# Performance work log

Measured on AMD Instinct MI355X. Metric: run time of the kernel, lower is better.

The kernel has to match this reference:

```python
import jax, jax.numpy as jnp
import numpy as np

N = 100000      # nodes
E = 3200000     # edges (avg degree 32)
F_IN = 500      # PubMed node features
H = 16          # hidden
C = 3           # PubMed classes


def setup_inputs() -> dict:
    key = jax.random.key(0)
    k1, k2, k3, k4, k5, k6 = jax.random.split(key, 6)
    x = jax.random.normal(k1, (N, F_IN), dtype=jnp.float32)
    edge_index = jax.random.randint(k2, (2, E), 0, N, dtype=jnp.int32)
    # GCNConv weights (glorot-ish scale) and zero biases
    W1 = jax.random.normal(k3, (F_IN, H), dtype=jnp.float32) * np.float32(np.sqrt(2.0 / (F_IN + H)))
    b1 = jnp.zeros((H,), dtype=jnp.float32)
    W2 = jax.random.normal(k4, (H, C), dtype=jnp.float32) * np.float32(np.sqrt(2.0 / (H + C)))
    b2 = jnp.zeros((C,), dtype=jnp.float32)
    return {"x": x, "W1": W1, "b1": b1, "W2": W2, "b2": b2, "edge_index": edge_index}


def gcn_layer(x, W, b, src, dst, n):
    # GCNConv: linear transform, add self-loops, symmetric degree normalization, scatter-add
    h = x @ W                                   # [N, F_out]
    loop = jnp.arange(n, dtype=src.dtype)
    s = jnp.concatenate([src, loop])            # [E+N]
    d = jnp.concatenate([dst, loop])            # [E+N]
    deg = jax.ops.segment_sum(jnp.ones_like(d, dtype=h.dtype), d, num_segments=n)
    dinv = jax.lax.rsqrt(jnp.maximum(deg, 1.0))  # deg >= 1 due to self-loops
    norm = dinv[s] * dinv[d]                    # [E+N]
    out = jax.ops.segment_sum(h[s] * norm[:, None], d, num_segments=n)
    return out + b


def reference(x, W1, b1, W2, b2, edge_index):
    src, dst = edge_index[0], edge_index[1]
    h = gcn_layer(x, W1, b1, src, dst, N)
    h = jax.nn.relu(h)
    # F.dropout in eval mode (reference is deterministic) is identity
    out = gcn_layer(h, W2, b2, src, dst, N)
    return jax.nn.log_softmax(out, axis=1)
```

## Files before the change

kernel.cpp:

```cpp
#include <hip/hip_runtime.h>
#include <hip/hip_fp16.h>
#include <math.h>

#define N_NODES 100000
#define N_EDGES 3200000
#define F_INF   500
#define H_DIM   16
#define C_DIM   3

#define NB      782
#define CAP     4608
#define GPAD    16
#define EPB     16384
#define NBLK_PART ((N_EDGES + EPB - 1) / EPB)

#define OFF_GCUR  0
#define OFF_DINV  12512
#define OFF_PAIRS 112512
#define OFF_ROWS  3715968
#define OFF_H1H   3816064
#define OFF_H2H   4616064

typedef float        f32x4 __attribute__((ext_vector_type(4)));
typedef unsigned int u32x4 __attribute__((ext_vector_type(4)));
typedef unsigned int u32x2 __attribute__((ext_vector_type(2)));

template <typename T>
__device__ inline T ntload(const T* p) { return __builtin_nontemporal_load(p); }
template <typename T>
__device__ inline void ntstore(T* p, T v) { __builtin_nontemporal_store(v, p); }

__device__ inline float2 h2f(unsigned u) {
    __half2 h = *reinterpret_cast<__half2*>(&u);
    return __half22float2(h);
}
__device__ inline unsigned f2h(float a, float b) {
    __half2 h = __floats2half2_rn(a, b);
    return *reinterpret_cast<unsigned*>(&h);
}

__global__ void k_init(int* __restrict__ gcur) {
    int b = blockIdx.x * 256 + threadIdx.x;
    if (b < NB) gcur[b * GPAD] = b * CAP;
}

__global__ __launch_bounds__(512) void k_part(const int* __restrict__ src,
                                              const int* __restrict__ dst,
                                              int* __restrict__ gcur,
                                              unsigned int* __restrict__ pairs) {
    __shared__ unsigned sbuf[EPB];
    __shared__ int lcnt[NB];
    __shared__ int lbase[NB];
    __shared__ int lstart[NB];
    __shared__ int lrank[NB];
    __shared__ int wtot[8];
    int t = threadIdx.x;
    int wid = t >> 6, lane = t & 63;
    int e0 = blockIdx.x * EPB;
    for (int i = t; i < NB; i += 512) { lcnt[i] = 0; lrank[i] = 0; }
    __syncthreads();
    for (int i = t; i < EPB; i += 512) {
        int e = e0 + i;
        if (e < N_EDGES) atomicAdd(&lcnt[ntload(dst + e) >> 7], 1);
    }
    __syncthreads();
    for (int b = t; b < NB; b += 512) {
        int c = lcnt[b];
        lbase[b] = c ? atomicAdd(&gcur[b * GPAD], c) : 0;
    }
    {
        int b0 = wid * 128 + lane * 2;
        int c0 = (b0 < NB) ? lcnt[b0] : 0;
        int c1 = (b0 + 1 < NB) ? lcnt[b0 + 1] : 0;
        int s = c0 + c1;
        int inc = s;
        for (int o = 1; o < 64; o <<= 1) { int y = __shfl_up(inc, o); if (lane >= o) inc += y; }
        if (lane == 63) wtot[wid] = inc;
        int excl = inc - s;
        if (b0 < NB) lstart[b0] = excl;
        if (b0 + 1 < NB) lstart[b0 + 1] = excl + c0;
    }
    __syncthreads();
    if (t == 0) { int r = 0; for (int w = 0; w < 8; ++w) { int v = wtot[w]; wtot[w] = r; r += v; } }
    __syncthreads();
    {
        int b0 = wid * 128 + lane * 2;
        int add = wtot[wid];
        if (b0 < NB) lstart[b0] += add;
        if (b0 + 1 < NB) lstart[b0 + 1] += add;
    }
    __syncthreads();
    for (int i = t; i < EPB; i += 512) {
        int e = e0 + i;
        if (e < N_EDGES) {
            int d = ntload(dst + e);
            int b = d >> 7;
            int r = atomicAdd(&lrank[b], 1);
            sbuf[lstart[b] + r] = ((unsigned)ntload(src + e) << 7) | (unsigned)(d & 127);
        }
    }
    __syncthreads();
    for (int b = wid; b < NB; b += 8) {
        int c = lcnt[b], ls = lstart[b], gb = lbase[b];
        int lim = (b + 1) * CAP;
        for (int i = lane; i < c; i += 64) {
            int pos = gb + i;
            if (pos < lim)
                pairs[pos] = sbuf[ls + i];
        }
    }
}

__global__ __launch_bounds__(512) void k_sort(unsigned int* __restrict__ pairs,
                                              const int* __restrict__ gcur,
                                              float* __restrict__ dinv,
                                              int* __restrict__ rows) {
    __shared__ unsigned sbuf[CAP];
    __shared__ unsigned sout[CAP];
    __shared__ int cnt[128];
    __shared__ int start[128];
    __shared__ int rank[128];
    int b = blockIdx.x, t = threadIdx.x;
    if (t < 128) { cnt[t] = 0; rank[t] = 0; }
    __syncthreads();
    int base = b * CAP;
    int n = min(gcur[b * GPAD] - base, CAP);
    for (int i = t; i < n; i += 512) {
        unsigned p = ntload(pairs + base + i);
        sbuf[i] = p;
        atomicAdd(&cnt[p & 127], 1);
    }
    __syncthreads();
    if (t < 64) {
        int c0 = cnt[2 * t], c1 = cnt[2 * t + 1];
        int s = c0 + c1;
        int inc = s;
        for (int o = 1; o < 64; o <<= 1) { int y = __shfl_up(inc, o); if (t >= o) inc += y; }
        int excl = inc - s;
        start[2 * t] = excl;
        start[2 * t + 1] = excl + c0;
        rows[b * 128 + 2 * t]     = (excl << 16) | c0;
        rows[b * 128 + 2 * t + 1] = ((excl + c0) << 16) | c1;
    }
    if (t >= 64 && t < 192) {
        int l = t - 64;
        int v = b * 128 + l;
        if (v < N_NODES) dinv[v] = rsqrtf((float)(cnt[l] + 1));
    }
    __syncthreads();
    for (int i = t; i < n; i += 512) {
        unsigned p = sbuf[i];
        int k = p & 127;
        int r = atomicAdd(&rank[k], 1);
        sout[start[k] + r] = p;
    }
    __syncthreads();
    for (int i = t; i < n; i += 512) ntstore(pairs + base + i, sout[i]);
}

#define KTILE 60
#define KSTRIDE 61
__global__ __launch_bounds__(256) void k_gemm1(const float* __restrict__ x,
                                               const float* __restrict__ W1,
                                               const float* __restrict__ dinv,
                                               unsigned int* __restrict__ h1h) {
    __shared__ float xs[256 * KSTRIDE];
    int t = threadIdx.x;
    int row0 = blockIdx.x * 256;
    int row = row0 + t;
    float acc[16];
#pragma unroll
    for (int j = 0; j < 16; ++j) acc[j] = 0.f;
    int rr = t >> 4;
    int cc = t & 15;
    for (int k0 = 0; k0 < F_INF; k0 += KTILE) {
        int kw = F_INF - k0; if (kw > KTILE) kw = KTILE;
        int nf4 = kw >> 2;
        __syncthreads();
#pragma unroll
        for (int s = 0; s < 16; ++s) {
            int r = s * 16 + rr;
            int gr = row0 + r;
            if (cc < nf4 && gr < N_NODES) {
                f32x4 v = ntload(reinterpret_cast<const f32x4*>(x + (size_t)gr * F_INF + k0 + cc * 4));
                float* q = xs + r * KSTRIDE + cc * 4;
                q[0] = v.x; q[1] = v.y; q[2] = v.z; q[3] = v.w;
            }
        }
        __syncthreads();
        if (row < N_NODES) {
            for (int kk = 0; kk < kw; ++kk) {
                float xv = xs[t * KSTRIDE + kk];
                const float* Wk = W1 + (k0 + kk) * 16;
#pragma unroll
                for (int j = 0; j < 16; ++j) acc[j] = fmaf(xv, Wk[j], acc[j]);
            }
        }
    }
    if (row < N_NODES) {
        float dv = dinv[row];
        u32x4 o0, o1;
        o0.x = f2h(dv * acc[0],  dv * acc[1]);  o0.y = f2h(dv * acc[2],  dv * acc[3]);
        o0.z = f2h(dv * acc[4],  dv * acc[5]);  o0.w = f2h(dv * acc[6],  dv * acc[7]);
        o1.x = f2h(dv * acc[8],  dv * acc[9]);  o1.y = f2h(dv * acc[10], dv * acc[11]);
        o1.z = f2h(dv * acc[12], dv * acc[13]); o1.w = f2h(dv * acc[14], dv * acc[15]);
        u32x4* o = reinterpret_cast<u32x4*>(h1h + (size_t)row * 8);
        ntstore(o, o0);
        ntstore(o + 1, o1);
    }
}

__global__ __launch_bounds__(512) void k_agg1(const unsigned int* __restrict__ pairs,
                                              const int* __restrict__ rows,
                                              const float* __restrict__ dinv,
                                              const unsigned int* __restrict__ h1h,
                                              const float* __restrict__ b1,
                                              const float* __restrict__ W2,
                                              unsigned int* __restrict__ h2h) {
    int b = blockIdx.x, t = threadIdx.x;
    int q = t & 3;
    int l = t >> 2;
    int v = b * 128 + l;
    if (v >= N_NODES) return;
    int e = rows[b * 128 + l];
    int st = b * CAP + (e >> 16);
    int cnt = e & 0xffff;
    int qo = q * 2;
    float dv = dinv[v];
    float s0 = 0.f, s1 = 0.f, s2 = 0.f, s3 = 0.f;
    int i = 0;
    for (; i + 8 <= cnt; i += 8) {
        unsigned p[8];
#pragma unroll
        for (int u = 0; u < 8; ++u) p[u] = ntload(pairs + st + i + u);
        u32x2 A[8];
#pragma unroll
        for (int u = 0; u < 8; ++u)
            A[u] = *reinterpret_cast<const u32x2*>(h1h + (size_t)(p[u] >> 7) * 8 + qo);
#pragma unroll
        for (int u = 0; u < 8; ++u) {
            float2 f0 = h2f(A[u].x), f1 = h2f(A[u].y);
            s0 += f0.x; s1 += f0.y; s2 += f1.x; s3 += f1.y;
        }
    }
    for (; i < cnt; ++i) {
        unsigned p = ntload(pairs + st + i);
        u32x2 A = *reinterpret_cast<const u32x2*>(h1h + (size_t)(p >> 7) * 8 + qo);
        float2 f0 = h2f(A.x), f1 = h2f(A.y);
        s0 += f0.x; s1 += f0.y; s2 += f1.x; s3 += f1.y;
    }
    u32x2 S = *reinterpret_cast<const u32x2*>(h1h + (size_t)v * 8 + qo);
    float2 t0 = h2f(S.x), t1 = h2f(S.y);
    f32x4 bb = reinterpret_cast<const f32x4*>(b1)[q];
    float a0 = fmaxf(fmaf(dv, s0 + t0.x, bb.x), 0.f);
    float a1 = fmaxf(fmaf(dv, s1 + t0.y, bb.y), 0.f);
    float a2 = fmaxf(fmaf(dv, s2 + t1.x, bb.z), 0.f);
    float a3 = fmaxf(fmaf(dv, s3 + t1.y, bb.w), 0.f);
    const float* Wq = W2 + q * 4 * 3;
    float c0 = fmaf(a0, Wq[0], fmaf(a1, Wq[3], fmaf(a2, Wq[6],  a3 * Wq[9])));
    float c1 = fmaf(a0, Wq[1], fmaf(a1, Wq[4], fmaf(a2, Wq[7],  a3 * Wq[10])));
    float c2 = fmaf(a0, Wq[2], fmaf(a1, Wq[5], fmaf(a2, Wq[8],  a3 * Wq[11])));
    c0 += __shfl_xor(c0, 1); c0 += __shfl_xor(c0, 2);
    c1 += __shfl_xor(c1, 1); c1 += __shfl_xor(c1, 2);
    c2 += __shfl_xor(c2, 1); c2 += __shfl_xor(c2, 2);
    if (q == 0) {
        u32x2 o;
        o.x = f2h(dv * c0, dv * c1);
        o.y = f2h(dv * c2, 0.f);
        ntstore(reinterpret_cast<u32x2*>(h2h) + v, o);
    }
}

__global__ __launch_bounds__(256) void k_agg2(const unsigned int* __restrict__ pairs,
                                              const int* __restrict__ rows,
                                              const float* __restrict__ dinv,
                                              const unsigned int* __restrict__ h2h,
                                              const float* __restrict__ b2,
                                              float* __restrict__ out) {
    int b = blockIdx.x, t = threadIdx.x;
    int half = t & 1;
    int l = t >> 1;
    int v = b * 128 + l;
    if (v >= N_NODES) return;
    int e = rows[b * 128 + l];
    int st = b * CAP + (e >> 16);
    int cnt = e & 0xffff;
    const u32x2* h2v = reinterpret_cast<const u32x2*>(h2h);
    float c0 = 0.f, c1 = 0.f, c2 = 0.f;
    int i = half;
    for (; i + 6 < cnt; i += 8) {
        unsigned p0 = ntload(pairs + st + i);
        unsigned p1 = ntload(pairs + st + i + 2);
        unsigned p2 = ntload(pairs + st + i + 4);
        unsigned p3 = ntload(pairs + st + i + 6);
        u32x2 A = h2v[p0 >> 7];
        u32x2 B = h2v[p1 >> 7];
        u32x2 C = h2v[p2 >> 7];
        u32x2 D = h2v[p3 >> 7];
        float2 f01, f2_;
        f01 = h2f(A.x); f2_ = h2f(A.y); c0 += f01.x; c1 += f01.y; c2 += f2_.x;
        f01 = h2f(B.x); f2_ = h2f(B.y); c0 += f01.x; c1 += f01.y; c2 += f2_.x;
        f01 = h2f(C.x); f2_ = h2f(C.y); c0 += f01.x; c1 += f01.y; c2 += f2_.x;
        f01 = h2f(D.x); f2_ = h2f(D.y); c0 += f01.x; c1 += f01.y; c2 += f2_.x;
    }
    for (; i < cnt; i += 2) {
        unsigned p = ntload(pairs + st + i);
        u32x2 A = h2v[p >> 7];
        float2 f01 = h2f(A.x), f2_ = h2f(A.y);
        c0 += f01.x; c1 += f01.y; c2 += f2_.x;
    }
    c0 += __shfl_xor(c0, 1);
    c1 += __shfl_xor(c1, 1);
    c2 += __shfl_xor(c2, 1);
    if (half == 0) {
        float dv = dinv[v];
        u32x2 hv = h2v[v];
        float2 f01 = h2f(hv.x), f2_ = h2f(hv.y);
        float z0 = fmaf(dv, c0 + f01.x, b2[0]);
        float z1 = fmaf(dv, c1 + f01.y, b2[1]);
        float z2 = fmaf(dv, c2 + f2_.x, b2[2]);
        float mx = fmaxf(z0, fmaxf(z1, z2));
        float lse = logf(expf(z0 - mx) + expf(z1 - mx) + expf(z2 - mx));
        out[v * 3 + 0] = z0 - mx - lse;
        out[v * 3 + 1] = z1 - mx - lse;
        out[v * 3 + 2] = z2 - mx - lse;
    }
}

extern "C" void kernel_launch(void* const* d_in, const int* in_sizes, int n_in,
                              void* d_out, int out_size, void* d_ws, size_t ws_size,
                              hipStream_t stream) {
    (void)in_sizes; (void)n_in; (void)out_size; (void)ws_size;
    const float* x  = (const float*)d_in[0];
    const float* W1 = (const float*)d_in[1];
    const float* b1 = (const float*)d_in[2];
    const float* W2 = (const float*)d_in[3];
    const float* b2 = (const float*)d_in[4];
    const int*   ei = (const int*)d_in[5];
    const int* src = ei;
    const int* dst = ei + N_EDGES;
    float* out = (float*)d_out;

    int* ws = (int*)d_ws;
    int*          gcur  = ws + OFF_GCUR;
    float*        dinv  = (float*)(ws + OFF_DINV);
    unsigned int* pairs = (unsigned int*)(ws + OFF_PAIRS);
    int*          rows  = ws + OFF_ROWS;
    unsigned int* h1h   = (unsigned int*)(ws + OFF_H1H);
    unsigned int* h2h   = (unsigned int*)(ws + OFF_H2H);

    k_init <<<(NB + 255) / 256, 256, 0, stream>>>(gcur);
    k_part <<<NBLK_PART, 512, 0, stream>>>(src, dst, gcur, pairs);
    k_sort <<<NB, 512, 0, stream>>>(pairs, gcur, dinv, rows);
    k_gemm1<<<(N_NODES + 255) / 256, 256, 0, stream>>>(x, W1, dinv, h1h);
    k_agg1 <<<NB, 512, 0, stream>>>(pairs, rows, dinv, h1h, b1, W2, h2h);
    k_agg2 <<<NB, 256, 0, stream>>>(pairs, rows, dinv, h2h, b2, out);
}
```

Before: 544.5 us.

## Register-prefetch next x tile in GEMM1 and shrink blocks to 128 rows

The first-layer GEMM kernel now loads the next K-tile of x into registers while the current tile in shared memory is being consumed, overlapping global loads with FMA work. Blocks shrink from 256 to 128 rows (782 blocks), which halves shared memory per block and should allow more resident blocks. The cost is 16 extra float4 registers per thread, which may reduce occupancy.

```diff
diff --git a/kernel.cpp b/kernel.cpp
--- a/kernel.cpp
+++ b/kernel.cpp
@@ -160,34 +160,52 @@
 
 #define KTILE 60
 #define KSTRIDE 61
-__global__ __launch_bounds__(256) void k_gemm1(const float* __restrict__ x,
+#define GROWS 128
+#define NTILE 9
+__global__ __launch_bounds__(128) void k_gemm1(const float* __restrict__ x,
                                                const float* __restrict__ W1,
                                                const float* __restrict__ dinv,
                                                unsigned int* __restrict__ h1h) {
-    __shared__ float xs[256 * KSTRIDE];
+    __shared__ float xs[GROWS * KSTRIDE];
     int t = threadIdx.x;
-    int row0 = blockIdx.x * 256;
+    int row0 = blockIdx.x * GROWS;
     int row = row0 + t;
-    float acc[16];
-#pragma unroll
-    for (int j = 0; j < 16; ++j) acc[j] = 0.f;
     int rr = t >> 4;
     int cc = t & 15;
-    for (int k0 = 0; k0 < F_INF; k0 += KTILE) {
-        int kw = F_INF - k0; if (kw > KTILE) kw = KTILE;
+    float acc[16];
+#pragma unroll
+    for (int j = 0; j < 16; ++j) acc[j] = 0.f;
+    f32x4 vreg[16];
+#pragma unroll
+    for (int s = 0; s < 16; ++s) {
+        int gr = row0 + s * 8 + rr;
+        if (cc < 15 && gr < N_NODES)
+            vreg[s] = ntload(reinterpret_cast<const f32x4*>(x + (size_t)gr * F_INF + cc * 4));
+    }
+    int k0 = 0;
+    for (int tile = 0; tile < NTILE; ++tile) {
+        int kw  = (tile < 8) ? KTILE : 20;
         int nf4 = kw >> 2;
         __syncthreads();
 #pragma unroll
         for (int s = 0; s < 16; ++s) {
-            int r = s * 16 + rr;
-            int gr = row0 + r;
-            if (cc < nf4 && gr < N_NODES) {
-                f32x4 v = ntload(reinterpret_cast<const f32x4*>(x + (size_t)gr * F_INF + k0 + cc * 4));
+            int r = s * 8 + rr;
+            if (cc < nf4 && row0 + r < N_NODES) {
                 float* q = xs + r * KSTRIDE + cc * 4;
-                q[0] = v.x; q[1] = v.y; q[2] = v.z; q[3] = v.w;
+                q[0] = vreg[s].x; q[1] = vreg[s].y; q[2] = vreg[s].z; q[3] = vreg[s].w;
             }
         }
         __syncthreads();
+        if (tile < NTILE - 1) {
+            int nk0  = k0 + KTILE;
+            int nnf4 = (tile < 7) ? 15 : 5;
+#pragma unroll
+            for (int s = 0; s < 16; ++s) {
+                int gr = row0 + s * 8 + rr;
+                if (cc < nnf4 && gr < N_NODES)
+                    vreg[s] = ntload(reinterpret_cast<const f32x4*>(x + (size_t)gr * F_INF + nk0 + cc * 4));
+            }
+        }
         if (row < N_NODES) {
             for (int kk = 0; kk < kw; ++kk) {
                 float xv = xs[t * KSTRIDE + kk];
@@ -196,6 +214,7 @@
                 for (int j = 0; j < 16; ++j) acc[j] = fmaf(xv, Wk[j], acc[j]);
             }
         }
+        k0 += KTILE;
     }
     if (row < N_NODES) {
         float dv = dinv[row];
@@ -352,7 +371,7 @@
     k_init <<<(NB + 255) / 256, 256, 0, stream>>>(gcur);
     k_part <<<NBLK_PART, 512, 0, stream>>>(src, dst, gcur, pairs);
     k_sort <<<NB, 512, 0, stream>>>(pairs, gcur, dinv, rows);
-    k_gemm1<<<(N_NODES + 255) / 256, 256, 0, stream>>>(x, W1, dinv, h1h);
+    k_gemm1<<<NB, GROWS, 0, stream>>>(x, W1, dinv, h1h);
     k_agg1 <<<NB, 512, 0, stream>>>(pairs, rows, dinv, h1h, b1, W2, h2h);
     k_agg2 <<<NB, 256, 0, stream>>>(pairs, rows, dinv, h2h, b2, out);
 }
```

New measurement: 531.2 us. -2.4%, faster.
